# Optimization experiments

Measured on AMD Instinct MI355X. Metric: run time of the kernel, lower is better.

Reference implementation:

```python
import jax, jax.numpy as jnp
import numpy as np

D, HS, HE, E, K = 1024, 2048, 1024, 8, 2   # d_model, shared hidden (d_ff//2), expert hidden (d_ff//4), n_experts, top_k
B, T = 4, 1024
N_SHARED = 1


def setup_inputs() -> dict:
    key = jax.random.key(0)
    ks = jax.random.split(key, 9)
    g = lambda k, shape, s: jax.random.normal(k, shape, jnp.float32) * s
    return {
        "x": g(ks[0], (B, T, D), 1.0),
        "t_emb": g(ks[1], (B, D), 1.0),
        "router_W": g(ks[2], (2 * D, E), 0.01),      # torch Linear(2C->E, bias=False), std=0.01 init
        "router_bias": jnp.zeros((E,), jnp.float32),  # load-balance bias buffer
        "w1": g(ks[3], (D, HS), 0.02),                # shared expert SwiGLU
        "w3": g(ks[4], (D, HS), 0.02),
        "w2": g(ks[5], (HS, D), 0.02),
        "W1e": g(ks[6], (E, D, HE), 0.02),            # routed experts, Linear->GELU->Linear
        "W2e": g(ks[7], (E, HE, D), 0.02),
    }


def reference(x, t_emb, router_W, router_bias, w1, w3, w2, W1e, W2e):
    Bb, Tt, C = x.shape
    xf = x.reshape(-1, C)                                              # [N, C]
    tf = jnp.broadcast_to(t_emb[:, None, :], (Bb, Tt, C)).reshape(-1, C)
    N = xf.shape[0]

    shared = (jax.nn.silu(xf @ w1) * (xf @ w3)) @ w2                   # [N, C]

    # router affinity (sigmoid, fp32)
    s = jax.nn.sigmoid((jnp.concatenate([xf, tf], axis=-1) @ router_W).astype(jnp.float32))
    sel_scores = s + router_bias                                       # [N, E]
    _, topk_idx = jax.lax.top_k(sel_scores, K)                         # [N, K]

    # gates normalized over selected raw affinities
    s_sel = jnp.take_along_axis(s, topk_idx, axis=1)                   # [N, K]
    denom = s_sel.sum(axis=1, keepdims=True)
    gates = jnp.where(denom > 1e-9, s_sel / (denom + 1e-9), 1.0 / K).astype(x.dtype)

    # combine weights [N, E]: scatter gates to selected experts
    combine = jnp.zeros((N, E), x.dtype).at[jnp.arange(N)[:, None], topk_idx].add(gates)

    # dense expert evaluation (reference form of grouped GEMM + scatter-combine)
    h = jax.nn.gelu(jnp.einsum('nc,ech->enh', xf, W1e), approximate=False)  # [E, N, He]
    y = jnp.einsum('enh,ehc->enc', h, W2e)                                   # [E, N, C]
    routed = jnp.einsum('ne,enc->nc', combine, y)                            # [N, C]

    return ((shared + routed) / (N_SHARED + K)).reshape(Bb, Tt, C)
```

## Files before the change

kernel.cpp:

```cpp
#include <hip/hip_runtime.h>
#include <hip/hip_bf16.h>
#include <math.h>

#define D_MODEL 1024
#define HS 2048
#define HE 1024
#define NEXP 8
#define NTOK 4096
#define NSLOT 8192

typedef __attribute__((ext_vector_type(4))) float f32x4;
typedef __attribute__((ext_vector_type(8))) short bf16x8;

__device__ __forceinline__ short f2b(float f) {
  __hip_bfloat16 h = __float2bfloat16(f);
  return *reinterpret_cast<short*>(&h);
}
__device__ __forceinline__ float b2f(short s) {
  return __bfloat162float(*reinterpret_cast<__hip_bfloat16*>(&s));
}

__device__ __forceinline__ void gl_lds16(const short* g, short* l) {
  __builtin_amdgcn_global_load_lds(
      (const __attribute__((address_space(1))) void*)g,
      (__attribute__((address_space(3))) void*)l, 16, 0, 0);
}

__device__ __forceinline__ void tr_tile(const float* __restrict__ in,
                                        short* __restrict__ out, int R, int C,
                                        int bx, int by, int bz, int rmap,
                                        float (*tile)[69], int t) {
  const int c0 = bx * 64;
  const int r0 = by * 64;
  const size_t bo = (size_t)bz * R * C;
  const int lr = t >> 4;
  const int lc4 = (t & 15) * 4;
#pragma unroll
  for (int i = 0; i < 4; i++) {
    const float4 v = *(const float4*)&in[bo + (size_t)(r0 + lr + i * 16) * C + c0 + lc4];
    tile[lc4 + 0][lr + i * 16] = v.x;
    tile[lc4 + 1][lr + i * 16] = v.y;
    tile[lc4 + 2][lr + i * 16] = v.z;
    tile[lc4 + 3][lr + i * 16] = v.w;
  }
  __syncthreads();
#pragma unroll
  for (int i = 0; i < 4; i++) {
    const int oc = (t >> 4) + i * 16;
    const int or4 = (t & 15) * 4;
    short4 o;
    o.x = f2b(tile[oc][or4 + 0]);
    o.y = f2b(tile[oc][or4 + 1]);
    o.z = f2b(tile[oc][or4 + 2]);
    o.w = f2b(tile[oc][or4 + 3]);
    const int c = c0 + oc;
    size_t orow;
    if (rmap == 0) orow = bo + (size_t)c * R;
    else orow = (size_t)((c >> 5) * 64 + (rmap == 2 ? 32 : 0) + (c & 31)) * R;
    *(short4*)&out[orow + r0 + or4] = o;
  }
}

__global__ __launch_bounds__(256) void tr_all(
    const float* __restrict__ w1, const float* __restrict__ w3,
    const float* __restrict__ w2, const float* __restrict__ W1e,
    const float* __restrict__ W2e, short* __restrict__ w13I,
    short* __restrict__ w2T, short* __restrict__ W1eT, short* __restrict__ W2eT) {
  __shared__ float tile[64][69];
  const int id = blockIdx.x;
  const int t = threadIdx.x;
  if (id < 1024) {
    const int z = id >> 9, rem = id & 511;
    tr_tile(z ? w3 : w1, w13I, D_MODEL, HS, rem & 31, rem >> 5, 0, z ? 2 : 1, tile, t);
  } else if (id < 1536) {
    const int rem = id - 1024;
    tr_tile(w2, w2T, HS, D_MODEL, rem & 15, rem >> 4, 0, 0, tile, t);
  } else {
    const int rem = id - 1536;
    const int z = rem >> 8, r2 = rem & 255;
    if (z < 8)
      tr_tile(W1e, W1eT, D_MODEL, HE, r2 & 15, r2 >> 4, z, 0, tile, t);
    else
      tr_tile(W2e, W2eT, HE, D_MODEL, r2 & 15, r2 >> 4, z - 8, 0, tile, t);
  }
}

__global__ __launch_bounds__(256) void router_kernel(
    const float* __restrict__ x, const float* __restrict__ temb,
    const float* __restrict__ rw, const float* __restrict__ rbias,
    short* __restrict__ xb, int* __restrict__ topk, float* __restrict__ gates) {
  const int t = (blockIdx.x * 256 + threadIdx.x) >> 6;
  const int lane = threadIdx.x & 63;
  const float* xr = x + (size_t)t * D_MODEL;
  const float* tr = temb + (size_t)(t >> 10) * D_MODEL;
  float acc[NEXP] = {};
#pragma unroll
  for (int i = 0; i < 4; i++) {
    const int j = i * 256 + lane * 4;
    const float4 xv = *(const float4*)&xr[j];
    const float4 tv = *(const float4*)&tr[j];
    short4 o;
    o.x = f2b(xv.x); o.y = f2b(xv.y); o.z = f2b(xv.z); o.w = f2b(xv.w);
    *(short4*)&xb[(size_t)t * D_MODEL + j] = o;
    const float* wx = rw + (size_t)j * NEXP;
    const float* wt = rw + (size_t)(D_MODEL + j) * NEXP;
    const float xa[4] = {xv.x, xv.y, xv.z, xv.w};
    const float ta[4] = {tv.x, tv.y, tv.z, tv.w};
#pragma unroll
    for (int u = 0; u < 4; u++)
#pragma unroll
      for (int e = 0; e < NEXP; e++)
        acc[e] += xa[u] * wx[u * NEXP + e] + ta[u] * wt[u * NEXP + e];
  }
#pragma unroll
  for (int off = 32; off; off >>= 1)
#pragma unroll
    for (int e = 0; e < NEXP; e++) acc[e] += __shfl_xor(acc[e], off);
  if (lane == 0) {
    float s[NEXP], sel[NEXP];
#pragma unroll
    for (int e = 0; e < NEXP; e++) {
      s[e] = 1.f / (1.f + expf(-acc[e]));
      sel[e] = s[e] + rbias[e];
    }
    int i0 = 0;
#pragma unroll
    for (int e = 1; e < NEXP; e++) if (sel[e] > sel[i0]) i0 = e;
    int i1 = (i0 == 0) ? 1 : 0;
#pragma unroll
    for (int e = 0; e < NEXP; e++) if (e != i0 && sel[e] > sel[i1]) i1 = e;
    float s0 = s[i0], s1 = s[i1], den = s0 + s1;
    float g0, g1;
    if (den > 1e-9f) { g0 = s0 / (den + 1e-9f); g1 = s1 / (den + 1e-9f); }
    else { g0 = 0.5f; g1 = 0.5f; }
    topk[t * 2] = i0; topk[t * 2 + 1] = i1;
    gates[t * 2] = g0; gates[t * 2 + 1] = g1;
  }
}

__global__ __launch_bounds__(1024) void group_kernel(const int* __restrict__ topk,
                                                     int* __restrict__ perm,
                                                     int* __restrict__ offs,
                                                     int* __restrict__ te,
                                                     int* __restrict__ tm,
                                                     int* __restrict__ ntile) {
  __shared__ int cnt[NEXP], cur[NEXP];
  const int t = threadIdx.x;
  if (t < NEXP) cnt[t] = 0;
  __syncthreads();
  int mye[8];
#pragma unroll
  for (int i = 0; i < 8; i++) {
    mye[i] = topk[i * 1024 + t];
    atomicAdd(&cnt[mye[i]], 1);
  }
  __syncthreads();
  if (t == 0) {
    int a = 0;
    for (int e = 0; e < NEXP; e++) { offs[e] = a; cur[e] = a; a += cnt[e]; }
    offs[NEXP] = a;
    int nt = 0;
    for (int e = 0; e < NEXP; e++)
      for (int m0 = 0; m0 < cnt[e]; m0 += 128) { te[nt] = e; tm[nt] = m0; nt++; }
    ntile[0] = nt;
  }
  __syncthreads();
#pragma unroll
  for (int i = 0; i < 8; i++) {
    int pos = atomicAdd(&cur[mye[i]], 1);
    perm[pos] = i * 1024 + t;
  }
}

__global__ __launch_bounds__(256, 2) void moe_k1(
    const short* __restrict__ xb, const short* __restrict__ w13I,
    const short* __restrict__ W1eT, short* __restrict__ ubuf,
    short* __restrict__ hexpb, const int* __restrict__ perm,
    const int* __restrict__ offs, const int* __restrict__ te,
    const int* __restrict__ tm, const int* __restrict__ ntile) {
  extern __shared__ short lds[];
  const int td = threadIdx.x;
  const int id = blockIdx.x;
  const bool isG1 = id < 512;
  int m_panel = 0, n_panel = 0, m0 = 0, rbeg = 0, rend = 0, bxn = 0;
  const short* Bb;
  if (isG1) {
    const int x = id & 7, w = id >> 3;
    n_panel = x * 2 + (w >> 5);
    m_panel = w & 31;
    Bb = w13I + (size_t)n_panel * 256 * 1024;
  } else {
    const int g = id - 512;
    const int ty = g >> 2;
    if (ty >= ntile[0]) return;
    bxn = g & 3;
    const int e = te[ty];
    m0 = tm[ty];
    rbeg = offs[e]; rend = offs[e + 1];
    Bb = W1eT + ((size_t)e * 1024 + bxn * 256) * 1024;
  }

  const int srow = td >> 2;
  const int scol = ((td & 3) ^ ((srow >> 1) & 3)) * 8;
  const short* ap[2];
  const short* bp[4];
#pragma unroll
  for (int i = 0; i < 2; i++) {
    const int row = i * 64 + srow;
    int grow;
    if (isG1) grow = m_panel * 128 + row;
    else grow = perm[min(rbeg + m0 + row, rend - 1)] >> 1;
    ap[i] = xb + (size_t)grow * 1024 + scol;
  }
#pragma unroll
  for (int u = 0; u < 4; u++) bp[u] = Bb + (size_t)(u * 64 + srow) * 1024 + scol;

#define K1STAGE(t_, b_)                                                \
  do {                                                                 \
    gl_lds16(ap[0] + (t_) * 32, lds + (b_) * 12288 + td * 8);          \
    gl_lds16(ap[1] + (t_) * 32, lds + (b_) * 12288 + 2048 + td * 8);   \
    gl_lds16(bp[0] + (t_) * 32, lds + (b_) * 12288 + 4096 + td * 8);   \
    gl_lds16(bp[1] + (t_) * 32, lds + (b_) * 12288 + 6144 + td * 8);   \
    gl_lds16(bp[2] + (t_) * 32, lds + (b_) * 12288 + 8192 + td * 8);   \
    gl_lds16(bp[3] + (t_) * 32, lds + (b_) * 12288 + 10240 + td * 8);  \
  } while (0)

  const int l = td & 63;
  const int wv = td >> 6;
  const int wm = wv >> 1;
  const int wn = wv & 1;
  const int lr = l & 15;
  const int kg = l >> 4;
  const int gsw = (kg ^ ((lr >> 1) & 3)) * 8;

#define LDA1(mf_) (*(const bf16x8*)&Ah[(unsigned)((wm * 64 + (mf_)*16 + lr) * 32) + gsw])
#define LDB1(nf_) (*(const bf16x8*)&Bh[(unsigned)((wn * 128 + (nf_)*16 + lr) * 32) + gsw])

  f32x4 acc[4][8] = {};

  K1STAGE(0, 0);
  asm volatile("s_waitcnt vmcnt(0)" ::: "memory");
  __builtin_amdgcn_s_barrier();

  for (int t = 0; t < 32; ++t) {
    const int p = t & 1, q = p ^ 1;
    const short* Ah = lds + p * 12288;
    const short* Bh = lds + p * 12288 + 4096;
    if (t < 31) {
      K1STAGE(t + 1, q);
      asm volatile("s_waitcnt vmcnt(6)" ::: "memory");
    } else {
      asm volatile("s_waitcnt vmcnt(0)" ::: "memory");
    }
    __builtin_amdgcn_s_barrier();
    {
      bf16x8 bf[8], af[4];
#pragma unroll
      for (int nf = 0; nf < 8; nf++) bf[nf] = LDB1(nf);
#pragma unroll
      for (int mf = 0; mf < 4; mf++) af[mf] = LDA1(mf);
      __builtin_amdgcn_s_setprio(1);
#pragma unroll
      for (int mf = 0; mf < 4; mf++)
#pragma unroll
        for (int nf = 0; nf < 8; nf++)
          acc[mf][nf] = __builtin_amdgcn_mfma_f32_16x16x32_bf16(af[mf], bf[nf],
                                                                acc[mf][nf], 0, 0, 0);
      __builtin_amdgcn_s_setprio(0);
    }
    __builtin_amdgcn_sched_barrier(0);
    __builtin_amdgcn_s_barrier();
  }

  const int rq = kg * 4;
  if (isG1) {
#pragma unroll
    for (int mf = 0; mf < 4; mf++)
#pragma unroll
      for (int j = 0; j < 4; j++) {
        const int row = m_panel * 128 + wm * 64 + mf * 16 + rq + j;
        short* Up = ubuf + (size_t)row * HS + n_panel * 128 + wn * 64;
#pragma unroll
        for (int pi = 0; pi < 4; pi++) {
          const int nf = (pi & 1) + (pi >> 1) * 4;
          const float a = acc[mf][nf][j];
          const float b = acc[mf][nf + 2][j];
          Up[(nf >> 2) * 32 + (nf & 1) * 16 + lr] = f2b(a / (1.f + expf(-a)) * b);
        }
      }
  } else {
#pragma unroll
    for (int mf = 0; mf < 4; mf++)
#pragma unroll
      for (int j = 0; j < 4; j++) {
        const int gi = rbeg + m0 + wm * 64 + mf * 16 + rq + j;
        if (gi < rend) {
          short* Cp = hexpb + (size_t)gi * HE + bxn * 256 + wn * 128 + lr;
#pragma unroll
          for (int nf = 0; nf < 8; nf++) {
            const float v = acc[mf][nf][j];
            Cp[nf * 16] = f2b(0.5f * v * (1.0f + erff(v * 0.70710678118654752f)));
          }
        }
      }
  }
#undef K1STAGE
#undef LDA1
#undef LDB1
}

__global__ __launch_bounds__(256, 2) void moe_k2(
    const short* __restrict__ ubuf, const short* __restrict__ w2T,
    const short* __restrict__ hexpb, const short* __restrict__ W2eT,
    float* __restrict__ out, short* __restrict__ yb,
    const int* __restrict__ perm, const int* __restrict__ offs,
    const float* __restrict__ gates, const int* __restrict__ te,
    const int* __restrict__ tm, const int* __restrict__ ntile) {
  extern __shared__ short lds[];
  const int td = threadIdx.x;
  const int id = blockIdx.x;
  const int l = td & 63;
  const int wv = td >> 6;
  const int lr = l & 15;

  if (id < 256) {
    const int xcd = id & 7, slot = id >> 3;
    const int n_panel = slot & 7;
    const int m_panel = xcd * 4 + (slot >> 3);
    const short* A = ubuf;
    const short* Bb = w2T + (size_t)n_panel * 128 * HS;

    const int srow = td >> 3;
    const int colsw8 = ((td & 7) ^ (srow & 7)) * 8;
    const short* ap[4];
    const short* bp[4];
#pragma unroll
    for (int u = 0; u < 4; u++) {
      const int trow = u * 32 + srow;
      ap[u] = A + (size_t)(m_panel * 128 + trow) * HS + colsw8;
      bp[u] = Bb + (size_t)trow * HS + colsw8;
    }
#define K2STAGE(t_, b_)                                                    \
  do {                                                                     \
    gl_lds16(ap[0] + (t_) * 64, lds + (b_) * 16384 + td * 8);              \
    gl_lds16(ap[1] + (t_) * 64, lds + (b_) * 16384 + 2048 + td * 8);       \
    gl_lds16(ap[2] + (t_) * 64, lds + (b_) * 16384 + 4096 + td * 8);       \
    gl_lds16(ap[3] + (t_) * 64, lds + (b_) * 16384 + 6144 + td * 8);       \
    gl_lds16(bp[0] + (t_) * 64, lds + (b_) * 16384 + 8192 + td * 8);       \
    gl_lds16(bp[1] + (t_) * 64, lds + (b_) * 16384 + 10240 + td * 8);      \
    gl_lds16(bp[2] + (t_) * 64, lds + (b_) * 16384 + 12288 + td * 8);      \
    gl_lds16(bp[3] + (t_) * 64, lds + (b_) * 16384 + 14336 + td * 8);      \
  } while (0)
    const int wm = (wv >> 1) * 64, wn = (wv & 1) * 64;
    const int swzk0 = ((0 + (l >> 4) * 16) ^ ((l & 7) << 4)) >> 1;
    const int swzk1 = ((64 + (l >> 4) * 16) ^ ((l & 7) << 4)) >> 1;
#define LDA2(mf_, swz_) (*(const bf16x8*)&Ah[(unsigned)(((mf_)*16 + lr) * 64) + (swz_)])
#define LDB2(nf_, swz_) (*(const bf16x8*)&Bh[(unsigned)(((nf_)*16 + lr) * 64) + (swz_)])
#define MM2(mf_, a_)                                                                   \
  acc[mf_][0] = __builtin_amdgcn_mfma_f32_16x16x32_bf16(a_, b0, acc[mf_][0], 0, 0, 0); \
  acc[mf_][1] = __builtin_amdgcn_mfma_f32_16x16x32_bf16(a_, b1, acc[mf_][1], 0, 0, 0); \
  acc[mf_][2] = __builtin_amdgcn_mfma_f32_16x16x32_bf16(a_, b2, acc[mf_][2], 0, 0, 0); \
  acc[mf_][3] = __builtin_amdgcn_mfma_f32_16x16x32_bf16(a_, b3, acc[mf_][3], 0, 0, 0)
    f32x4 acc[4][4] = {};
    K2STAGE(0, 0);
    for (int t = 0; t < 32; ++t) {
      const int p = t & 1, q = p ^ 1;
      const short* Ah = lds + p * 16384 + wm * 64;
      const short* Bh = lds + p * 16384 + 8192 + wn * 64;
      if (t < 31) {
        K2STAGE(t + 1, q);
        asm volatile("s_waitcnt vmcnt(8)" ::: "memory");
      } else {
        asm volatile("s_waitcnt vmcnt(0)" ::: "memory");
      }
      __builtin_amdgcn_s_barrier();
      {
        bf16x8 b0, b1, b2, b3, a0, a1, a2, a3;
        b0 = LDB2(0, swzk0); b1 = LDB2(1, swzk0); b2 = LDB2(2, swzk0); b3 = LDB2(3, swzk0);
        a0 = LDA2(0, swzk0); a1 = LDA2(1, swzk0); a2 = LDA2(2, swzk0); a3 = LDA2(3, swzk0);
        __builtin_amdgcn_s_setprio(1);
        MM2(0, a0); MM2(1, a1); MM2(2, a2); MM2(3, a3);
        __builtin_amdgcn_s_setprio(0);
        b0 = LDB2(0, swzk1); b1 = LDB2(1, swzk1); b2 = LDB2(2, swzk1); b3 = LDB2(3, swzk1);
        a0 = LDA2(0, swzk1); a1 = LDA2(1, swzk1); a2 = LDA2(2, swzk1); a3 = LDA2(3, swzk1);
        __builtin_amdgcn_s_setprio(1);
        MM2(0, a0); MM2(1, a1); MM2(2, a2); MM2(3, a3);
        __builtin_amdgcn_s_setprio(0);
      }
      __builtin_amdgcn_sched_barrier(0);
      __builtin_amdgcn_s_barrier();
    }
    const int rq = (l >> 4) * 4;
#pragma unroll
    for (int mf = 0; mf < 4; mf++)
#pragma unroll
      for (int j = 0; j < 4; j++) {
        const int tok = m_panel * 128 + wm + mf * 16 + rq + j;
        float* Op = out + (size_t)tok * D_MODEL + n_panel * 128 + wn + lr;
#pragma unroll
        for (int nf = 0; nf < 4; nf++) Op[nf * 16] = acc[mf][nf][j];
      }
#undef K2STAGE
#undef LDA2
#undef LDB2
#undef MM2
  } else {
    const int g = id - 256;
    const int ty = g >> 2;
    if (ty >= ntile[0]) return;
    const int bxn = g & 3;
    const int e = te[ty];
    const int m0 = tm[ty];
    const int rbeg = offs[e], rend = offs[e + 1];
    const short* Bb = W2eT + ((size_t)e * 1024 + bxn * 256) * 1024;

    const int srow = td >> 2;
    const int scol = ((td & 3) ^ ((srow >> 1) & 3)) * 8;
    const short* ap[2];
    const short* bp[4];
#pragma unroll
    for (int i = 0; i < 2; i++) {
      const int grow = min(rbeg + m0 + i * 64 + srow, rend - 1);
      ap[i] = hexpb + (size_t)grow * 1024 + scol;
    }
#pragma unroll
    for (int u = 0; u < 4; u++) bp[u] = Bb + (size_t)(u * 64 + srow) * 1024 + scol;

#define G2STAGE(t_, b_)                                                \
  do {                                                                 \
    gl_lds16(ap[0] + (t_) * 32, lds + (b_) * 12288 + td * 8);          \
    gl_lds16(ap[1] + (t_) * 32, lds + (b_) * 12288 + 2048 + td * 8);   \
    gl_lds16(bp[0] + (t_) * 32, lds + (b_) * 12288 + 4096 + td * 8);   \
    gl_lds16(bp[1] + (t_) * 32, lds + (b_) * 12288 + 6144 + td * 8);   \
    gl_lds16(bp[2] + (t_) * 32, lds + (b_) * 12288 + 8192 + td * 8);   \
    gl_lds16(bp[3] + (t_) * 32, lds + (b_) * 12288 + 10240 + td * 8);  \
  } while (0)
    const int wm = wv >> 1;
    const int wn = wv & 1;
    const int kg = l >> 4;
    const int gsw = (kg ^ ((lr >> 1) & 3)) * 8;
#define LDA3(mf_) (*(const bf16x8*)&Ah[(unsigned)((wm * 64 + (mf_)*16 + lr) * 32) + gsw])
#define LDB3(nf_) (*(const bf16x8*)&Bh[(unsigned)((wn * 128 + (nf_)*16 + lr) * 32) + gsw])
    f32x4 acc[4][8] = {};
    G2STAGE(0, 0);
    asm volatile("s_waitcnt vmcnt(0)" ::: "memory");
    __builtin_amdgcn_s_barrier();
    for (int t = 0; t < 32; ++t) {
      const int p = t & 1, q = p ^ 1;
      const short* Ah = lds + p * 12288;
      const short* Bh = lds + p * 12288 + 4096;
      if (t < 31) {
        G2STAGE(t + 1, q);
        asm volatile("s_waitcnt vmcnt(6)" ::: "memory");
      } else {
        asm volatile("s_waitcnt vmcnt(0)" ::: "memory");
      }
      __builtin_amdgcn_s_barrier();
      {
        bf16x8 bf[8], af[4];
#pragma unroll
        for (int nf = 0; nf < 8; nf++) bf[nf] = LDB3(nf);
#pragma unroll
        for (int mf = 0; mf < 4; mf++) af[mf] = LDA3(mf);
        __builtin_amdgcn_s_setprio(1);
#pragma unroll
        for (int mf = 0; mf < 4; mf++)
#pragma unroll
          for (int nf = 0; nf < 8; nf++)
            acc[mf][nf] = __builtin_amdgcn_mfma_f32_16x16x32_bf16(af[mf], bf[nf],
                                                                  acc[mf][nf], 0, 0, 0);
        __builtin_amdgcn_s_setprio(0);
      }
      __builtin_amdgcn_sched_barrier(0);
      __builtin_amdgcn_s_barrier();
    }
    const int rq = kg * 4;
#pragma unroll
    for (int mf = 0; mf < 4; mf++)
#pragma unroll
      for (int j = 0; j < 4; j++) {
        const int gi = rbeg + m0 + wm * 64 + mf * 16 + rq + j;
        if (gi < rend) {
          const int slot = perm[gi];
          const float gt = gates[slot];
          short* Cp = yb + (size_t)slot * D_MODEL + bxn * 256 + wn * 128 + lr;
#pragma unroll
          for (int nf = 0; nf < 8; nf++) Cp[nf * 16] = f2b(gt * acc[mf][nf][j]);
        }
      }
#undef G2STAGE
#undef LDA3
#undef LDB3
  }
}

__global__ __launch_bounds__(256) void combine_kernel(float* __restrict__ out,
                                                      const short* __restrict__ yb) {
  const float inv3 = 1.0f / 3.0f;
#pragma unroll
  for (int rep = 0; rep < 2; rep++) {
    const int i = (rep * 2048 + blockIdx.x) * 256 + threadIdx.x;
    const int base = i * 4;
    const int tok = base >> 10;
    const int col = base & (D_MODEL - 1);
    float4 s = *(float4*)&out[base];
    const short4 y0 = *(const short4*)&yb[(size_t)(tok * 2) * D_MODEL + col];
    const short4 y1 = *(const short4*)&yb[(size_t)(tok * 2 + 1) * D_MODEL + col];
    s.x = (s.x + b2f(y0.x) + b2f(y1.x)) * inv3;
    s.y = (s.y + b2f(y0.y) + b2f(y1.y)) * inv3;
    s.z = (s.z + b2f(y0.z) + b2f(y1.z)) * inv3;
    s.w = (s.w + b2f(y0.w) + b2f(y1.w)) * inv3;
    *(float4*)&out[base] = s;
  }
}

extern "C" void kernel_launch(void* const* d_in, const int* in_sizes, int n_in,
                              void* d_out, int out_size, void* d_ws, size_t ws_size,
                              hipStream_t stream) {
  const float* x = (const float*)d_in[0];
  const float* temb = (const float*)d_in[1];
  const float* rw = (const float*)d_in[2];
  const float* rbias = (const float*)d_in[3];
  const float* w1 = (const float*)d_in[4];
  const float* w3 = (const float*)d_in[5];
  const float* w2 = (const float*)d_in[6];
  const float* W1e = (const float*)d_in[7];
  const float* W2e = (const float*)d_in[8];
  float* out = (float*)d_out;

  const size_t MB = 1ull << 20;
  char* w = (char*)d_ws;
  short* xb    = (short*)(w + 0 * MB);
  short* w13I  = (short*)(w + 8 * MB);
  short* w2T   = (short*)(w + 16 * MB);
  short* W1eT  = (short*)(w + 20 * MB);
  short* W2eT  = (short*)(w + 36 * MB);
  short* ubuf  = (short*)(w + 52 * MB);
  short* hexpb = (short*)(w + 68 * MB);
  short* yb    = (short*)(w + 84 * MB);
  float* gates = (float*)(w + 100 * MB);
  int* topk    = (int*)(w + 100 * MB + 32 * 1024);
  int* perm    = (int*)(w + 100 * MB + 64 * 1024);
  int* meta    = (int*)(w + 100 * MB + 96 * 1024);
  int* offs    = meta;
  int* te      = meta + 16;
  int* tm      = meta + 128;
  int* ntile   = meta + 256;

  hipFuncSetAttribute((const void*)&moe_k1,
                      hipFuncAttributeMaxDynamicSharedMemorySize, 49152);
  hipFuncSetAttribute((const void*)&moe_k2,
                      hipFuncAttributeMaxDynamicSharedMemorySize, 65536);

  tr_all<<<5632, 256, 0, stream>>>(w1, w3, w2, W1e, W2e, w13I, w2T, W1eT, W2eT);
  router_kernel<<<NTOK / 4, 256, 0, stream>>>(x, temb, rw, rbias, xb, topk, gates);
  group_kernel<<<1, 1024, 0, stream>>>(topk, perm, offs, te, tm, ntile);

  moe_k1<<<800, 256, 49152, stream>>>(xb, w13I, W1eT, ubuf, hexpb, perm, offs,
                                      te, tm, ntile);

  moe_k2<<<544, 256, 65536, stream>>>(ubuf, w2T, hexpb, W2eT, out, yb, perm,
                                      offs, gates, te, tm, ntile);

  combine_kernel<<<2048, 256, 0, stream>>>(out, yb);
}
```

Before: 216.9 us.

## Shrink GEMM tiles, triple-buffer k1, split expert down-proj and fuse combine into shared GEMM

Halves the N tile of the first-stage GEMMs (128x128 instead of 128x256), doubling the block count and raising the occupancy hint to 3, with a 3-stage LDS ring pipeline that prefetches two K-steps ahead. The routed down-projection moves into its own kernel with the same smaller-tile pipeline, launched before the shared down-projection. The shared down-projection kernel now reads the gated expert outputs and does the final combine and divide in its epilogue, which removes the separate combine pass and the extra fp32 round-trip of out. The cost is more blocks re-reading the A operand, and two serialized kernels where the shared and routed down-projections previously ran together in one launch.

New measurement: 215.4 us. About the same (-0.7%).

```diff
diff --git a/kernel.cpp b/kernel.cpp
--- a/kernel.cpp
+++ b/kernel.cpp
@@ -172,7 +172,8 @@
   }
 }
 
-__global__ __launch_bounds__(256, 2) void moe_k1(
+
+__global__ __launch_bounds__(256, 3) void moe_k1(
     const short* __restrict__ xb, const short* __restrict__ w13I,
     const short* __restrict__ W1eT, short* __restrict__ ubuf,
     short* __restrict__ hexpb, const int* __restrict__ perm,
@@ -181,29 +182,29 @@
   extern __shared__ short lds[];
   const int td = threadIdx.x;
   const int id = blockIdx.x;
-  const bool isG1 = id < 512;
+  const bool isG1 = id < 1024;
   int m_panel = 0, n_panel = 0, m0 = 0, rbeg = 0, rend = 0, bxn = 0;
   const short* Bb;
   if (isG1) {
     const int x = id & 7, w = id >> 3;
-    n_panel = x * 2 + (w >> 5);
+    n_panel = x * 4 + (w >> 5);
     m_panel = w & 31;
-    Bb = w13I + (size_t)n_panel * 256 * 1024;
+    Bb = w13I + (size_t)n_panel * 128 * 1024;
   } else {
-    const int g = id - 512;
-    const int ty = g >> 2;
+    const int g = id - 1024;
+    const int ty = g >> 3;
     if (ty >= ntile[0]) return;
-    bxn = g & 3;
+    bxn = g & 7;
     const int e = te[ty];
     m0 = tm[ty];
     rbeg = offs[e]; rend = offs[e + 1];
-    Bb = W1eT + ((size_t)e * 1024 + bxn * 256) * 1024;
+    Bb = W1eT + ((size_t)e * 1024 + bxn * 128) * 1024;
   }
 
   const int srow = td >> 2;
   const int scol = ((td & 3) ^ ((srow >> 1) & 3)) * 8;
   const short* ap[2];
-  const short* bp[4];
+  const short* bp[2];
 #pragma unroll
   for (int i = 0; i < 2; i++) {
     const int row = i * 64 + srow;
@@ -211,65 +212,60 @@
     if (isG1) grow = m_panel * 128 + row;
     else grow = perm[min(rbeg + m0 + row, rend - 1)] >> 1;
     ap[i] = xb + (size_t)grow * 1024 + scol;
-  }
-#pragma unroll
-  for (int u = 0; u < 4; u++) bp[u] = Bb + (size_t)(u * 64 + srow) * 1024 + scol;
-
-#define K1STAGE(t_, b_)                                                \
-  do {                                                                 \
-    gl_lds16(ap[0] + (t_) * 32, lds + (b_) * 12288 + td * 8);          \
-    gl_lds16(ap[1] + (t_) * 32, lds + (b_) * 12288 + 2048 + td * 8);   \
-    gl_lds16(bp[0] + (t_) * 32, lds + (b_) * 12288 + 4096 + td * 8);   \
-    gl_lds16(bp[1] + (t_) * 32, lds + (b_) * 12288 + 6144 + td * 8);   \
-    gl_lds16(bp[2] + (t_) * 32, lds + (b_) * 12288 + 8192 + td * 8);   \
-    gl_lds16(bp[3] + (t_) * 32, lds + (b_) * 12288 + 10240 + td * 8);  \
+    bp[i] = Bb + (size_t)row * 1024 + scol;
+  }
+
+#define STG(t_, b_)                                                  \
+  do {                                                               \
+    gl_lds16(ap[0] + (t_) * 32, lds + (b_) * 8192 + td * 8);         \
+    gl_lds16(ap[1] + (t_) * 32, lds + (b_) * 8192 + 2048 + td * 8);  \
+    gl_lds16(bp[0] + (t_) * 32, lds + (b_) * 8192 + 4096 + td * 8);  \
+    gl_lds16(bp[1] + (t_) * 32, lds + (b_) * 8192 + 6144 + td * 8);  \
   } while (0)
 
   const int l = td & 63;
   const int wv = td >> 6;
-  const int wm = wv >> 1;
-  const int wn = wv & 1;
+  const int wm = wv >> 1, wn = wv & 1;
   const int lr = l & 15;
   const int kg = l >> 4;
   const int gsw = (kg ^ ((lr >> 1) & 3)) * 8;
 
 #define LDA1(mf_) (*(const bf16x8*)&Ah[(unsigned)((wm * 64 + (mf_)*16 + lr) * 32) + gsw])
-#define LDB1(nf_) (*(const bf16x8*)&Bh[(unsigned)((wn * 128 + (nf_)*16 + lr) * 32) + gsw])
-
-  f32x4 acc[4][8] = {};
-
-  K1STAGE(0, 0);
-  asm volatile("s_waitcnt vmcnt(0)" ::: "memory");
+#define LDB1(nf_) (*(const bf16x8*)&Bh[(unsigned)((wn * 64 + (nf_)*16 + lr) * 32) + gsw])
+
+  f32x4 acc[4][4] = {};
+
+  STG(0, 0); STG(1, 1);
+  asm volatile("s_waitcnt vmcnt(4)" ::: "memory");
   __builtin_amdgcn_s_barrier();
 
+  int pb = 0, sb = 2;
   for (int t = 0; t < 32; ++t) {
-    const int p = t & 1, q = p ^ 1;
-    const short* Ah = lds + p * 12288;
-    const short* Bh = lds + p * 12288 + 4096;
-    if (t < 31) {
-      K1STAGE(t + 1, q);
-      asm volatile("s_waitcnt vmcnt(6)" ::: "memory");
-    } else {
-      asm volatile("s_waitcnt vmcnt(0)" ::: "memory");
-    }
-    __builtin_amdgcn_s_barrier();
+    const short* Ah = lds + pb * 8192;
+    const short* Bh = lds + pb * 8192 + 4096;
+    const bool st = (t + 2 < 32);
+    if (st) STG(t + 2, sb);
     {
-      bf16x8 bf[8], af[4];
-#pragma unroll
-      for (int nf = 0; nf < 8; nf++) bf[nf] = LDB1(nf);
+      bf16x8 af[4], bf[4];
+#pragma unroll
+      for (int nf = 0; nf < 4; nf++) bf[nf] = LDB1(nf);
 #pragma unroll
       for (int mf = 0; mf < 4; mf++) af[mf] = LDA1(mf);
       __builtin_amdgcn_s_setprio(1);
 #pragma unroll
       for (int mf = 0; mf < 4; mf++)
 #pragma unroll
-        for (int nf = 0; nf < 8; nf++)
+        for (int nf = 0; nf < 4; nf++)
           acc[mf][nf] = __builtin_amdgcn_mfma_f32_16x16x32_bf16(af[mf], bf[nf],
                                                                 acc[mf][nf], 0, 0, 0);
       __builtin_amdgcn_s_setprio(0);
     }
     __builtin_amdgcn_sched_barrier(0);
+    if (st) asm volatile("s_waitcnt vmcnt(4)" ::: "memory");
+    else    asm volatile("s_waitcnt vmcnt(0)" ::: "memory");
     __builtin_amdgcn_s_barrier();
+    pb = (pb == 2) ? 0 : pb + 1;
+    sb = (sb == 2) ? 0 : sb + 1;
   }
 
   const int rq = kg * 4;
@@ -279,13 +275,12 @@
 #pragma unroll
       for (int j = 0; j < 4; j++) {
         const int row = m_panel * 128 + wm * 64 + mf * 16 + rq + j;
-        short* Up = ubuf + (size_t)row * HS + n_panel * 128 + wn * 64;
-#pragma unroll
-        for (int pi = 0; pi < 4; pi++) {
-          const int nf = (pi & 1) + (pi >> 1) * 4;
+        short* Up = ubuf + (size_t)row * HS + (n_panel * 2 + wn) * 32;
+#pragma unroll
+        for (int nf = 0; nf < 2; nf++) {
           const float a = acc[mf][nf][j];
           const float b = acc[mf][nf + 2][j];
-          Up[(nf >> 2) * 32 + (nf & 1) * 16 + lr] = f2b(a / (1.f + expf(-a)) * b);
+          Up[nf * 16 + lr] = f2b(a / (1.f + expf(-a)) * b);
         }
       }
   } else {
@@ -295,51 +290,142 @@
       for (int j = 0; j < 4; j++) {
         const int gi = rbeg + m0 + wm * 64 + mf * 16 + rq + j;
         if (gi < rend) {
-          short* Cp = hexpb + (size_t)gi * HE + bxn * 256 + wn * 128 + lr;
-#pragma unroll
-          for (int nf = 0; nf < 8; nf++) {
+          short* Cp = hexpb + (size_t)gi * HE + bxn * 128 + wn * 64 + lr;
+#pragma unroll
+          for (int nf = 0; nf < 4; nf++) {
             const float v = acc[mf][nf][j];
             Cp[nf * 16] = f2b(0.5f * v * (1.0f + erff(v * 0.70710678118654752f)));
           }
         }
       }
   }
-#undef K1STAGE
+#undef STG
 #undef LDA1
 #undef LDB1
 }
 
-__global__ __launch_bounds__(256, 2) void moe_k2(
+__global__ __launch_bounds__(256, 3) void moe_gg2(
+    const short* __restrict__ hexpb, const short* __restrict__ W2eT,
+    short* __restrict__ yb, const int* __restrict__ perm,
+    const int* __restrict__ offs, const float* __restrict__ gates,
+    const int* __restrict__ te, const int* __restrict__ tm,
+    const int* __restrict__ ntile) {
+  extern __shared__ short lds[];
+  const int td = threadIdx.x;
+  const int g = blockIdx.x;
+  const int ty = g >> 3;
+  if (ty >= ntile[0]) return;
+  const int bxn = g & 7;
+  const int e = te[ty];
+  const int m0 = tm[ty];
+  const int rbeg = offs[e], rend = offs[e + 1];
+  const short* Bb = W2eT + ((size_t)e * 1024 + bxn * 128) * 1024;
+
+  const int srow = td >> 2;
+  const int scol = ((td & 3) ^ ((srow >> 1) & 3)) * 8;
+  const short* ap[2];
+  const short* bp[2];
+#pragma unroll
+  for (int i = 0; i < 2; i++) {
+    const int grow = min(rbeg + m0 + i * 64 + srow, rend - 1);
+    ap[i] = hexpb + (size_t)grow * 1024 + scol;
+    bp[i] = Bb + (size_t)(i * 64 + srow) * 1024 + scol;
+  }
+
+#define STG(t_, b_)                                                  \
+  do {                                                               \
+    gl_lds16(ap[0] + (t_) * 32, lds + (b_) * 8192 + td * 8);         \
+    gl_lds16(ap[1] + (t_) * 32, lds + (b_) * 8192 + 2048 + td * 8);  \
+    gl_lds16(bp[0] + (t_) * 32, lds + (b_) * 8192 + 4096 + td * 8);  \
+    gl_lds16(bp[1] + (t_) * 32, lds + (b_) * 8192 + 6144 + td * 8);  \
+  } while (0)
+
+  const int l = td & 63;
+  const int wv = td >> 6;
+  const int wm = wv >> 1, wn = wv & 1;
+  const int lr = l & 15;
+  const int kg = l >> 4;
+  const int gsw = (kg ^ ((lr >> 1) & 3)) * 8;
+
+#define LDA1(mf_) (*(const bf16x8*)&Ah[(unsigned)((wm * 64 + (mf_)*16 + lr) * 32) + gsw])
+#define LDB1(nf_) (*(const bf16x8*)&Bh[(unsigned)((wn * 64 + (nf_)*16 + lr) * 32) + gsw])
+
+  f32x4 acc[4][4] = {};
+
+  STG(0, 0); STG(1, 1);
+  asm volatile("s_waitcnt vmcnt(4)" ::: "memory");
+  __builtin_amdgcn_s_barrier();
+
+  int pb = 0, sb = 2;
+  for (int t = 0; t < 32; ++t) {
+    const short* Ah = lds + pb * 8192;
+    const short* Bh = lds + pb * 8192 + 4096;
+    const bool st = (t + 2 < 32);
+    if (st) STG(t + 2, sb);
+    {
+      bf16x8 af[4], bf[4];
+#pragma unroll
+      for (int nf = 0; nf < 4; nf++) bf[nf] = LDB1(nf);
+#pragma unroll
+      for (int mf = 0; mf < 4; mf++) af[mf] = LDA1(mf);
+      __builtin_amdgcn_s_setprio(1);
+#pragma unroll
+      for (int mf = 0; mf < 4; mf++)
+#pragma unroll
+        for (int nf = 0; nf < 4; nf++)
+          acc[mf][nf] = __builtin_amdgcn_mfma_f32_16x16x32_bf16(af[mf], bf[nf],
+                                                                acc[mf][nf], 0, 0, 0);
+      __builtin_amdgcn_s_setprio(0);
+    }
+    __builtin_amdgcn_sched_barrier(0);
+    if (st) asm volatile("s_waitcnt vmcnt(4)" ::: "memory");
+    else    asm volatile("s_waitcnt vmcnt(0)" ::: "memory");
+    __builtin_amdgcn_s_barrier();
+    pb = (pb == 2) ? 0 : pb + 1;
+    sb = (sb == 2) ? 0 : sb + 1;
+  }
+
+  const int rq = kg * 4;
+#pragma unroll
+  for (int mf = 0; mf < 4; mf++)
+#pragma unroll
+    for (int j = 0; j < 4; j++) {
+      const int gi = rbeg + m0 + wm * 64 + mf * 16 + rq + j;
+      if (gi < rend) {
+        const int slot = perm[gi];
+        const float gt = gates[slot];
+        short* Cp = yb + (size_t)slot * D_MODEL + bxn * 128 + wn * 64 + lr;
+#pragma unroll
+        for (int nf = 0; nf < 4; nf++) Cp[nf * 16] = f2b(gt * acc[mf][nf][j]);
+      }
+    }
+#undef STG
+#undef LDA1
+#undef LDB1
+}
+
+__global__ __launch_bounds__(256, 2) void moe_g2(
     const short* __restrict__ ubuf, const short* __restrict__ w2T,
-    const short* __restrict__ hexpb, const short* __restrict__ W2eT,
-    float* __restrict__ out, short* __restrict__ yb,
-    const int* __restrict__ perm, const int* __restrict__ offs,
-    const float* __restrict__ gates, const int* __restrict__ te,
-    const int* __restrict__ tm, const int* __restrict__ ntile) {
+    const short* __restrict__ yb, float* __restrict__ out) {
   extern __shared__ short lds[];
   const int td = threadIdx.x;
   const int id = blockIdx.x;
-  const int l = td & 63;
-  const int wv = td >> 6;
-  const int lr = l & 15;
-
-  if (id < 256) {
-    const int xcd = id & 7, slot = id >> 3;
-    const int n_panel = slot & 7;
-    const int m_panel = xcd * 4 + (slot >> 3);
-    const short* A = ubuf;
-    const short* Bb = w2T + (size_t)n_panel * 128 * HS;
-
-    const int srow = td >> 3;
-    const int colsw8 = ((td & 7) ^ (srow & 7)) * 8;
-    const short* ap[4];
-    const short* bp[4];
-#pragma unroll
-    for (int u = 0; u < 4; u++) {
-      const int trow = u * 32 + srow;
-      ap[u] = A + (size_t)(m_panel * 128 + trow) * HS + colsw8;
-      bp[u] = Bb + (size_t)trow * HS + colsw8;
-    }
+  const int xcd = id & 7, slot = id >> 3;
+  const int n_panel = slot & 7;
+  const int m_panel = xcd * 4 + (slot >> 3);
+  const short* Bb = w2T + (size_t)n_panel * 128 * HS;
+
+  const int srow = td >> 3;
+  const int colsw8 = ((td & 7) ^ (srow & 7)) * 8;
+  const short* ap[4];
+  const short* bp[4];
+#pragma unroll
+  for (int u = 0; u < 4; u++) {
+    const int trow = u * 32 + srow;
+    ap[u] = ubuf + (size_t)(m_panel * 128 + trow) * HS + colsw8;
+    bp[u] = Bb + (size_t)trow * HS + colsw8;
+  }
+
 #define K2STAGE(t_, b_)                                                    \
   do {                                                                     \
     gl_lds16(ap[0] + (t_) * 64, lds + (b_) * 16384 + td * 8);              \
@@ -351,9 +437,14 @@
     gl_lds16(bp[2] + (t_) * 64, lds + (b_) * 16384 + 12288 + td * 8);      \
     gl_lds16(bp[3] + (t_) * 64, lds + (b_) * 16384 + 14336 + td * 8);      \
   } while (0)
-    const int wm = (wv >> 1) * 64, wn = (wv & 1) * 64;
-    const int swzk0 = ((0 + (l >> 4) * 16) ^ ((l & 7) << 4)) >> 1;
-    const int swzk1 = ((64 + (l >> 4) * 16) ^ ((l & 7) << 4)) >> 1;
+
+  const int l = td & 63;
+  const int wv = td >> 6;
+  const int wm = (wv >> 1) * 64, wn = (wv & 1) * 64;
+  const int lr = l & 15;
+  const int swzk0 = ((0 + (l >> 4) * 16) ^ ((l & 7) << 4)) >> 1;
+  const int swzk1 = ((64 + (l >> 4) * 16) ^ ((l & 7) << 4)) >> 1;
+
 #define LDA2(mf_, swz_) (*(const bf16x8*)&Ah[(unsigned)(((mf_)*16 + lr) * 64) + (swz_)])
 #define LDB2(nf_, swz_) (*(const bf16x8*)&Bh[(unsigned)(((nf_)*16 + lr) * 64) + (swz_)])
 #define MM2(mf_, a_)                                                                   \
@@ -361,157 +452,57 @@
   acc[mf_][1] = __builtin_amdgcn_mfma_f32_16x16x32_bf16(a_, b1, acc[mf_][1], 0, 0, 0); \
   acc[mf_][2] = __builtin_amdgcn_mfma_f32_16x16x32_bf16(a_, b2, acc[mf_][2], 0, 0, 0); \
   acc[mf_][3] = __builtin_amdgcn_mfma_f32_16x16x32_bf16(a_, b3, acc[mf_][3], 0, 0, 0)
-    f32x4 acc[4][4] = {};
-    K2STAGE(0, 0);
-    for (int t = 0; t < 32; ++t) {
-      const int p = t & 1, q = p ^ 1;
-      const short* Ah = lds + p * 16384 + wm * 64;
-      const short* Bh = lds + p * 16384 + 8192 + wn * 64;
-      if (t < 31) {
-        K2STAGE(t + 1, q);
-        asm volatile("s_waitcnt vmcnt(8)" ::: "memory");
-      } else {
-        asm volatile("s_waitcnt vmcnt(0)" ::: "memory");
-      }
-      __builtin_amdgcn_s_barrier();
-      {
-        bf16x8 b0, b1, b2, b3, a0, a1, a2, a3;
-        b0 = LDB2(0, swzk0); b1 = LDB2(1, swzk0); b2 = LDB2(2, swzk0); b3 = LDB2(3, swzk0);
-        a0 = LDA2(0, swzk0); a1 = LDA2(1, swzk0); a2 = LDA2(2, swzk0); a3 = LDA2(3, swzk0);
-        __builtin_amdgcn_s_setprio(1);
-        MM2(0, a0); MM2(1, a1); MM2(2, a2); MM2(3, a3);
-        __builtin_amdgcn_s_setprio(0);
-        b0 = LDB2(0, swzk1); b1 = LDB2(1, swzk1); b2 = LDB2(2, swzk1); b3 = LDB2(3, swzk1);
-        a0 = LDA2(0, swzk1); a1 = LDA2(1, swzk1); a2 = LDA2(2, swzk1); a3 = LDA2(3, swzk1);
-        __builtin_amdgcn_s_setprio(1);
-        MM2(0, a0); MM2(1, a1); MM2(2, a2); MM2(3, a3);
-        __builtin_amdgcn_s_setprio(0);
-      }
-      __builtin_amdgcn_sched_barrier(0);
-      __builtin_amdgcn_s_barrier();
-    }
-    const int rq = (l >> 4) * 4;
-#pragma unroll
-    for (int mf = 0; mf < 4; mf++)
-#pragma unroll
-      for (int j = 0; j < 4; j++) {
-        const int tok = m_panel * 128 + wm + mf * 16 + rq + j;
-        float* Op = out + (size_t)tok * D_MODEL + n_panel * 128 + wn + lr;
-#pragma unroll
-        for (int nf = 0; nf < 4; nf++) Op[nf * 16] = acc[mf][nf][j];
-      }
+
+  f32x4 acc[4][4] = {};
+
+  K2STAGE(0, 0);
+  for (int t = 0; t < 32; ++t) {
+    const int p = t & 1, q = p ^ 1;
+    const short* Ah = lds + p * 16384 + wm * 64;
+    const short* Bh = lds + p * 16384 + 8192 + wn * 64;
+    if (t < 31) {
+      K2STAGE(t + 1, q);
+      asm volatile("s_waitcnt vmcnt(8)" ::: "memory");
+    } else {
+      asm volatile("s_waitcnt vmcnt(0)" ::: "memory");
+    }
+    __builtin_amdgcn_s_barrier();
+    {
+      bf16x8 b0, b1, b2, b3, a0, a1, a2, a3;
+      b0 = LDB2(0, swzk0); b1 = LDB2(1, swzk0); b2 = LDB2(2, swzk0); b3 = LDB2(3, swzk0);
+      a0 = LDA2(0, swzk0); a1 = LDA2(1, swzk0); a2 = LDA2(2, swzk0); a3 = LDA2(3, swzk0);
+      __builtin_amdgcn_s_setprio(1);
+      MM2(0, a0); MM2(1, a1); MM2(2, a2); MM2(3, a3);
+      __builtin_amdgcn_s_setprio(0);
+      b0 = LDB2(0, swzk1); b1 = LDB2(1, swzk1); b2 = LDB2(2, swzk1); b3 = LDB2(3, swzk1);
+      a0 = LDA2(0, swzk1); a1 = LDA2(1, swzk1); a2 = LDA2(2, swzk1); a3 = LDA2(3, swzk1);
+      __builtin_amdgcn_s_setprio(1);
+      MM2(0, a0); MM2(1, a1); MM2(2, a2); MM2(3, a3);
+      __builtin_amdgcn_s_setprio(0);
+    }
+    __builtin_amdgcn_sched_barrier(0);
+    __builtin_amdgcn_s_barrier();
+  }
+
+  const int rq = (l >> 4) * 4;
+  const float inv3 = 1.0f / 3.0f;
+#pragma unroll
+  for (int mf = 0; mf < 4; mf++)
+#pragma unroll
+    for (int j = 0; j < 4; j++) {
+      const int tok = m_panel * 128 + wm + mf * 16 + rq + j;
+      const int colb = n_panel * 128 + wn + lr;
+      const short* y0p = yb + (size_t)(tok * 2) * D_MODEL + colb;
+      const short* y1p = yb + (size_t)(tok * 2 + 1) * D_MODEL + colb;
+      float* Op = out + (size_t)tok * D_MODEL + colb;
+#pragma unroll
+      for (int nf = 0; nf < 4; nf++)
+        Op[nf * 16] = (acc[mf][nf][j] + b2f(y0p[nf * 16]) + b2f(y1p[nf * 16])) * inv3;
+    }
 #undef K2STAGE
 #undef LDA2
 #undef LDB2
 #undef MM2
-  } else {
-    const int g = id - 256;
-    const int ty = g >> 2;
-    if (ty >= ntile[0]) return;
-    const int bxn = g & 3;
-    const int e = te[ty];
-    const int m0 = tm[ty];
-    const int rbeg = offs[e], rend = offs[e + 1];
-    const short* Bb = W2eT + ((size_t)e * 1024 + bxn * 256) * 1024;
-
-    const int srow = td >> 2;
-    const int scol = ((td & 3) ^ ((srow >> 1) & 3)) * 8;
-    const short* ap[2];
-    const short* bp[4];
-#pragma unroll
-    for (int i = 0; i < 2; i++) {
-      const int grow = min(rbeg + m0 + i * 64 + srow, rend - 1);
-      ap[i] = hexpb + (size_t)grow * 1024 + scol;
-    }
-#pragma unroll
-    for (int u = 0; u < 4; u++) bp[u] = Bb + (size_t)(u * 64 + srow) * 1024 + scol;
-
-#define G2STAGE(t_, b_)                                                \
-  do {                                                                 \
-    gl_lds16(ap[0] + (t_) * 32, lds + (b_) * 12288 + td * 8);          \
-    gl_lds16(ap[1] + (t_) * 32, lds + (b_) * 12288 + 2048 + td * 8);   \
-    gl_lds16(bp[0] + (t_) * 32, lds + (b_) * 12288 + 4096 + td * 8);   \
-    gl_lds16(bp[1] + (t_) * 32, lds + (b_) * 12288 + 6144 + td * 8);   \
-    gl_lds16(bp[2] + (t_) * 32, lds + (b_) * 12288 + 8192 + td * 8);   \
-    gl_lds16(bp[3] + (t_) * 32, lds + (b_) * 12288 + 10240 + td * 8);  \
-  } while (0)
-    const int wm = wv >> 1;
-    const int wn = wv & 1;
-    const int kg = l >> 4;
-    const int gsw = (kg ^ ((lr >> 1) & 3)) * 8;
-#define LDA3(mf_) (*(const bf16x8*)&Ah[(unsigned)((wm * 64 + (mf_)*16 + lr) * 32) + gsw])
-#define LDB3(nf_) (*(const bf16x8*)&Bh[(unsigned)((wn * 128 + (nf_)*16 + lr) * 32) + gsw])
-    f32x4 acc[4][8] = {};
-    G2STAGE(0, 0);
-    asm volatile("s_waitcnt vmcnt(0)" ::: "memory");
-    __builtin_amdgcn_s_barrier();
-    for (int t = 0; t < 32; ++t) {
-      const int p = t & 1, q = p ^ 1;
-      const short* Ah = lds + p * 12288;
-      const short* Bh = lds + p * 12288 + 4096;
-      if (t < 31) {
-        G2STAGE(t + 1, q);
-        asm volatile("s_waitcnt vmcnt(6)" ::: "memory");
-      } else {
-        asm volatile("s_waitcnt vmcnt(0)" ::: "memory");
-      }
-      __builtin_amdgcn_s_barrier();
-      {
-        bf16x8 bf[8], af[4];
-#pragma unroll
-        for (int nf = 0; nf < 8; nf++) bf[nf] = LDB3(nf);
-#pragma unroll
-        for (int mf = 0; mf < 4; mf++) af[mf] = LDA3(mf);
-        __builtin_amdgcn_s_setprio(1);
-#pragma unroll
-        for (int mf = 0; mf < 4; mf++)
-#pragma unroll
-          for (int nf = 0; nf < 8; nf++)
-            acc[mf][nf] = __builtin_amdgcn_mfma_f32_16x16x32_bf16(af[mf], bf[nf],
-                                                                  acc[mf][nf], 0, 0, 0);
-        __builtin_amdgcn_s_setprio(0);
-      }
-      __builtin_amdgcn_sched_barrier(0);
-      __builtin_amdgcn_s_barrier();
-    }
-    const int rq = kg * 4;
-#pragma unroll
-    for (int mf = 0; mf < 4; mf++)
-#pragma unroll
-      for (int j = 0; j < 4; j++) {
-        const int gi = rbeg + m0 + wm * 64 + mf * 16 + rq + j;
-        if (gi < rend) {
-          const int slot = perm[gi];
-          const float gt = gates[slot];
-          short* Cp = yb + (size_t)slot * D_MODEL + bxn * 256 + wn * 128 + lr;
-#pragma unroll
-          for (int nf = 0; nf < 8; nf++) Cp[nf * 16] = f2b(gt * acc[mf][nf][j]);
-        }
-      }
-#undef G2STAGE
-#undef LDA3
-#undef LDB3
-  }
-}
-
-__global__ __launch_bounds__(256) void combine_kernel(float* __restrict__ out,
-                                                      const short* __restrict__ yb) {
-  const float inv3 = 1.0f / 3.0f;
-#pragma unroll
-  for (int rep = 0; rep < 2; rep++) {
-    const int i = (rep * 2048 + blockIdx.x) * 256 + threadIdx.x;
-    const int base = i * 4;
-    const int tok = base >> 10;
-    const int col = base & (D_MODEL - 1);
-    float4 s = *(float4*)&out[base];
-    const short4 y0 = *(const short4*)&yb[(size_t)(tok * 2) * D_MODEL + col];
-    const short4 y1 = *(const short4*)&yb[(size_t)(tok * 2 + 1) * D_MODEL + col];
-    s.x = (s.x + b2f(y0.x) + b2f(y1.x)) * inv3;
-    s.y = (s.y + b2f(y0.y) + b2f(y1.y)) * inv3;
-    s.z = (s.z + b2f(y0.z) + b2f(y1.z)) * inv3;
-    s.w = (s.w + b2f(y0.w) + b2f(y1.w)) * inv3;
-    *(float4*)&out[base] = s;
-  }
 }
 
 extern "C" void kernel_launch(void* const* d_in, const int* in_sizes, int n_in,
@@ -549,18 +540,20 @@
 
   hipFuncSetAttribute((const void*)&moe_k1,
                       hipFuncAttributeMaxDynamicSharedMemorySize, 49152);
-  hipFuncSetAttribute((const void*)&moe_k2,
+  hipFuncSetAttribute((const void*)&moe_gg2,
+                      hipFuncAttributeMaxDynamicSharedMemorySize, 49152);
+  hipFuncSetAttribute((const void*)&moe_g2,
                       hipFuncAttributeMaxDynamicSharedMemorySize, 65536);
 
   tr_all<<<5632, 256, 0, stream>>>(w1, w3, w2, W1e, W2e, w13I, w2T, W1eT, W2eT);
   router_kernel<<<NTOK / 4, 256, 0, stream>>>(x, temb, rw, rbias, xb, topk, gates);
   group_kernel<<<1, 1024, 0, stream>>>(topk, perm, offs, te, tm, ntile);
 
-  moe_k1<<<800, 256, 49152, stream>>>(xb, w13I, W1eT, ubuf, hexpb, perm, offs,
-                                      te, tm, ntile);
-
-  moe_k2<<<544, 256, 65536, stream>>>(ubuf, w2T, hexpb, W2eT, out, yb, perm,
-                                      offs, gates, te, tm, ntile);
-
-  combine_kernel<<<2048, 256, 0, stream>>>(out, yb);
-}
+  moe_k1<<<1600, 256, 49152, stream>>>(xb, w13I, W1eT, ubuf, hexpb, perm, offs,
+                                       te, tm, ntile);
+
+  moe_gg2<<<576, 256, 49152, stream>>>(hexpb, W2eT, yb, perm, offs, gates,
+                                       te, tm, ntile);
+
+  moe_g2<<<256, 256, 65536, stream>>>(ubuf, w2T, yb, out);
+}
```
